# Optimization experiments

Measured on AMD Instinct MI355X. Metric: run time of the kernel, lower is better.

## Reference

```python
import jax, jax.numpy as jnp
import numpy as np

# Module config (matches init_kwargs)
W_BIT = 2
PS_BIT = 8
IC = 256
OC = 256
K = 3
N_XBAR = 576
STRIDE = 1
PAD = 1
NUM_IC = min(IC, N_XBAR // (K * K))   # 64 input channels per crossbar array
GROUPS = IC // NUM_IC                 # 4 arrays (col_slide), ic divides evenly
QP_W = 2 ** W_BIT - 1                 # unsigned levels for nonneg pos/neg weights
QN_PS = -(2 ** (PS_BIT - 1))          # signed psum range
QP_PS = 2 ** (PS_BIT - 1) - 1


def lsq(v, s, qn, qp):
    """LSQ quantize-dequantize with straight-through rounding."""
    vs = jnp.clip(v / s, qn, qp)
    vbar = vs + jax.lax.stop_gradient(jnp.round(vs) - vs)
    return vbar * s


def conv2d(x, w):
    # x: [B, C, H, W], w: [O, C, k, k]
    return jax.lax.conv_general_dilated(
        x, w, window_strides=(STRIDE, STRIDE),
        padding=((PAD, PAD), (PAD, PAD)),
        dimension_numbers=('NCHW', 'OIHW', 'NCHW'))


def setup_inputs() -> dict:
    key = jax.random.key(0)
    k1, k2, k3, k4, k5 = jax.random.split(key, 5)
    x = jax.random.normal(k1, (16, IC, 56, 56), dtype=jnp.float32)
    weight = jax.random.normal(k2, (OC, IC, K, K), dtype=jnp.float32) * 0.05
    # positive LSQ step sizes, roughly 2*E|w|/sqrt(Qp) scale
    w_scale = jax.random.uniform(k3, (GROUPS,), dtype=jnp.float32) * 0.04 + 0.01
    ps_scale_p = jax.random.uniform(k4, (GROUPS,), dtype=jnp.float32) * 0.05 + 0.02
    ps_scale_n = jax.random.uniform(k5, (GROUPS,), dtype=jnp.float32) * 0.05 + 0.02
    return {"x": x, "weight": weight, "w_scale": w_scale,
            "ps_scale_p": ps_scale_p, "ps_scale_n": ps_scale_n}


def reference(x, weight, w_scale, ps_scale_p, ps_scale_n):
    B, _, H, W = x.shape
    # im2col tiling over input channels into GROUPS crossbar arrays
    xg = x.reshape(B, GROUPS, NUM_IC, H, W)                  # [B,G,cg,H,W]
    wg = weight.reshape(OC, GROUPS, NUM_IC, K, K)            # [O,G,cg,k,k]
    # pos / neg weight split, per-array LSQ weight quantization (shared quantizer)
    s_w = w_scale[:, None, None, None, None]                 # [G,1,1,1,1]
    wg_t = jnp.transpose(wg, (1, 0, 2, 3, 4))                # [G,O,cg,k,k]
    wq_p = lsq(jax.nn.relu(wg_t), s_w, 0, QP_W)
    wq_n = lsq(jax.nn.relu(-wg_t), s_w, 0, QP_W)
    xg_t = jnp.transpose(xg, (1, 0, 2, 3, 4))                # [G,B,cg,H,W]
    # per-array partial-sum convs (vmapped over arrays)
    vconv = jax.vmap(conv2d, in_axes=(0, 0))
    psum_p = vconv(xg_t, wq_p)                               # [G,B,O,h,w]
    psum_n = vconv(xg_t, wq_n)
    # per-array psum LSQ quantization ('Array' mode), then accumulate
    s_p = ps_scale_p[:, None, None, None, None]
    s_n = ps_scale_n[:, None, None, None, None]
    out_p = jnp.sum(lsq(psum_p, s_p, QN_PS, QP_PS), axis=0)  # [B,O,h,w]
    out_n = jnp.sum(lsq(psum_n, s_n, QN_PS, QP_PS), axis=0)
    return out_p - out_n
```

## Files before the change

kernel.cpp:

```cpp
#include <hip/hip_runtime.h>
#include <hip/hip_bf16.h>

typedef __attribute__((ext_vector_type(8))) short bf16x8_t;
typedef __attribute__((ext_vector_type(4))) float f32x4_t;
typedef __attribute__((ext_vector_type(4))) unsigned int u32x4_t;

#define XP_BYTES 55115776u
#define WT_BYTES 2359296u

typedef __attribute__((address_space(1))) const unsigned int ga_u32_t;
typedef __attribute__((address_space(3))) unsigned int lds_u32_t;

__device__ __forceinline__ void g2l16(const void* g, void* l) {
  __builtin_amdgcn_global_load_lds((ga_u32_t*)g, (lds_u32_t*)l, 16, 0, 0);
}

__global__ __launch_bounds__(256) void prep_x(const float* __restrict__ x,
                                              __hip_bfloat16* __restrict__ xp) {
  __shared__ float ls[64 * 57];
  int blk = blockIdx.x;
  int g = blk / 896;
  int r = blk - g * 896;
  int b = r / 56;
  int h = r - b * 56;
  int tid = threadIdx.x;
  const float* src = x + (size_t)(b * 256 + g * 64) * 3136 + h * 56;
  for (int i = tid; i < 64 * 56; i += 256) {
    int c = i / 56, w = i - c * 56;
    ls[c * 57 + w] = src[(size_t)c * 3136 + w];
  }
  __syncthreads();
  __hip_bfloat16* gbbase = xp + (size_t)(g * 16 + b) * 58 * 58 * 128;
  __hip_bfloat16* dst = gbbase + ((size_t)(h + 1) * 58 + 1) * 128;
  int wp = tid >> 7;
  int inner = tid & 127;
  int hl = inner >> 6, c = inner & 63;
  for (int w0 = 0; w0 < 56; w0 += 2) {
    int w = w0 + wp;
    float v = ls[c * 57 + w];
    __hip_bfloat16 hi = __float2bfloat16(v);
    __hip_bfloat16 val = hl ? __float2bfloat16(v - __bfloat162float(hi)) : hi;
    dst[(size_t)w * 128 + inner] = val;
  }
  __hip_bfloat16 z = __float2bfloat16(0.0f);
  {
    __hip_bfloat16* rowp = gbbase + (size_t)(h + 1) * 58 * 128;
    if (tid < 128) rowp[inner] = z;
    else           rowp[57 * 128 + inner] = z;
  }
  if (h == 0) {
    for (int i = tid; i < 58 * 128; i += 256) gbbase[i] = z;
  }
  if (h == 55) {
    __hip_bfloat16* r57 = gbbase + (size_t)57 * 58 * 128;
    for (int i = tid; i < 58 * 128; i += 256) r57[i] = z;
  }
}

__global__ __launch_bounds__(256) void prep_w(const float* __restrict__ wgt,
                                              const float* __restrict__ wsc,
                                              unsigned short* __restrict__ wtf) {
  int idx = blockIdx.x * 256 + threadIdx.x;
  if (idx >= 147456) return;
  int l = idx & 63;
  int ni = (idx >> 6) & 3;
  int wq = (idx >> 8) & 3;
  int u = idx >> 10;
  int g = u / 36;
  int r36 = u - g * 36;
  int sgn = (r36 >= 18) ? 1 : 0;
  int r18 = r36 - sgn * 18;
  int tap = r18 >> 1, cc = r18 & 1;
  int oc = wq * 64 + ni * 16 + (l & 15);
  float inv = 1.f / wsc[g];
  unsigned short pk[8];
#pragma unroll
  for (int e = 0; e < 8; ++e) {
    int c = cc * 32 + ((l >> 4) << 3) + e;
    float w = wgt[(size_t)oc * 2304 + (g * 64 + c) * 9 + tap] * inv;
    if (sgn) w = -w;
    float q = rintf(fminf(fmaxf(w, 0.f), 3.f));
    union { __hip_bfloat16 h; unsigned short s; } cv;
    cv.h = __float2bfloat16(q);
    pk[e] = cv.s;
  }
  u32x4_t v;
  v[0] = (unsigned)pk[0] | ((unsigned)pk[1] << 16);
  v[1] = (unsigned)pk[2] | ((unsigned)pk[3] << 16);
  v[2] = (unsigned)pk[4] | ((unsigned)pk[5] << 16);
  v[3] = (unsigned)pk[6] | ((unsigned)pk[7] << 16);
  *(u32x4_t*)(wtf + (size_t)idx * 8) = v;
}

#define MEMPIN asm volatile("" ::: "memory")
#define BAR __builtin_amdgcn_s_barrier()
#define VMCNT0 asm volatile("s_waitcnt vmcnt(0)" ::: "memory")

__global__ __launch_bounds__(256, 2) void conv_mfma(
    const unsigned short* __restrict__ xp, const unsigned short* __restrict__ wtf,
    const float* __restrict__ wsc, const float* __restrict__ psp,
    const float* __restrict__ psn, float* __restrict__ out) {
  __shared__ char Astrip[65536];

  const int bid = blockIdx.x;
  const int wg = (bid & 7) * 98 + (bid >> 3);
  const int b = wg / 49;
  const int t = wg - b * 49;
  const int r0 = (t << 6) / 56;

  const int tid = threadIdx.x;
  const int wv = tid >> 6;
  const int l = tid & 63;

  int pxb[4];
#pragma unroll
  for (int mi = 0; mi < 4; ++mi) {
    int m = (t << 6) + mi * 16 + (l & 15);
    int rv = m / 56, w = m - rv * 56;
    pxb[mi] = ((rv - r0) << 6) + w;
  }

  float w0s = wsc[0], w1s = wsc[1], w2s = wsc[2], w3s = wsc[3];
  float p0 = psp[0], p1 = psp[1], p2 = psp[2], p3 = psp[3];
  float n0 = psn[0], n1 = psn[1], n2 = psn[2], n3 = psn[3];

  f32x4_t acc[4][4], oacc[4][4];
  const f32x4_t fz = {0.f, 0.f, 0.f, 0.f};
#pragma unroll
  for (int i = 0; i < 4; ++i)
#pragma unroll
    for (int j = 0; j < 4; ++j) { acc[i][j] = fz; oacc[i][j] = fz; }

  const char* xg = (const char*)xp;
  const char* wtb = (const char*)wtf + (wv << 12) + (l << 4);
  const unsigned a_gbbase = (unsigned)((b * 3364 + r0 * 58) * 256);

#define STAGE_STRIP(gg)                                                        \
  {                                                                            \
    const char* s_ = xg + (unsigned)(gg)*13778944u + a_gbbase;                 \
    _Pragma("unroll")                                                          \
    for (int k_ = 0; k_ < 16; ++k_) {                                          \
      int idx_ = tid + (k_ << 8);                                              \
      int px_ = idx_ >> 4, sl_ = idx_ & 15;                                    \
      int sr_ = px_ >> 6, xc_ = px_ & 63;                                      \
      g2l16(s_ + (sr_ * 58 + xc_) * 256 +                                      \
                (((sl_ & 8) | ((sl_ & 7) ^ (xc_ & 7))) << 4),                  \
            Astrip + idx_ * 16);                                               \
    }                                                                          \
  }

#define LOADB(d0, d1, d2, d3, uu)                                              \
  {                                                                            \
    const char* p_ = wtb + (unsigned)(uu) * 16384u;                            \
    d0 = *(const bf16x8_t*)(p_);                                               \
    d1 = *(const bf16x8_t*)(p_ + 1024);                                        \
    d2 = *(const bf16x8_t*)(p_ + 2048);                                        \
    d3 = *(const bf16x8_t*)(p_ + 3072);                                        \
  }

#define READA(cc_, tyo_)                                                       \
  {                                                                            \
    const int kj_ = ((cc_) << 2) + (l >> 4);                                   \
    _Pragma("unroll")                                                          \
    for (int mi = 0; mi < 4; ++mi) {                                           \
      int px_ = pxb[mi] + (tyo_);                                              \
      int base_ = (px_ << 8) + ((kj_ ^ (px_ & 7)) << 4);                       \
      ahi[mi] = *(const bf16x8_t*)(Astrip + base_);                            \
      alo[mi] = *(const bf16x8_t*)(Astrip + base_ + 128);                      \
    }                                                                          \
  }

#define MMA32(B0, B1, B2, B3)                                                  \
  __builtin_amdgcn_s_setprio(1);                                               \
  _Pragma("unroll")                                                            \
  for (int mi = 0; mi < 4; ++mi) {                                             \
    acc[mi][0] = __builtin_amdgcn_mfma_f32_16x16x32_bf16(ahi[mi], B0, acc[mi][0], 0, 0, 0); \
    acc[mi][1] = __builtin_amdgcn_mfma_f32_16x16x32_bf16(ahi[mi], B1, acc[mi][1], 0, 0, 0); \
    acc[mi][2] = __builtin_amdgcn_mfma_f32_16x16x32_bf16(ahi[mi], B2, acc[mi][2], 0, 0, 0); \
    acc[mi][3] = __builtin_amdgcn_mfma_f32_16x16x32_bf16(ahi[mi], B3, acc[mi][3], 0, 0, 0); \
  }                                                                            \
  _Pragma("unroll")                                                            \
  for (int mi = 0; mi < 4; ++mi) {                                             \
    acc[mi][0] = __builtin_amdgcn_mfma_f32_16x16x32_bf16(alo[mi], B0, acc[mi][0], 0, 0, 0); \
    acc[mi][1] = __builtin_amdgcn_mfma_f32_16x16x32_bf16(alo[mi], B1, acc[mi][1], 0, 0, 0); \
    acc[mi][2] = __builtin_amdgcn_mfma_f32_16x16x32_bf16(alo[mi], B2, acc[mi][2], 0, 0, 0); \
    acc[mi][3] = __builtin_amdgcn_mfma_f32_16x16x32_bf16(alo[mi], B3, acc[mi][3], 0, 0, 0); \
  }                                                                            \
  __builtin_amdgcn_s_setprio(0);

#define QUANTIZE(gg, ss)                                                       \
  {                                                                            \
    float sw = ((gg) & 2) ? (((gg) & 1) ? w3s : w2s) : (((gg) & 1) ? w1s : w0s); \
    float sp = ((gg) & 2) ? (((gg) & 1) ? p3 : p2) : (((gg) & 1) ? p1 : p0);   \
    float sn = ((gg) & 2) ? (((gg) & 1) ? n3 : n2) : (((gg) & 1) ? n1 : n0);   \
    float sq = (ss) ? sn : sp;                                                 \
    float rs = sw / sq;                                                        \
    float sm = (ss) ? -sq : sq;                                                \
    _Pragma("unroll")                                                          \
    for (int mi = 0; mi < 4; ++mi)                                             \
      _Pragma("unroll")                                                        \
      for (int ni = 0; ni < 4; ++ni)                                           \
        _Pragma("unroll")                                                      \
        for (int j = 0; j < 4; ++j) {                                          \
          float v = acc[mi][ni][j] * rs;                                       \
          v = fminf(fmaxf(v, -128.f), 127.f);                                  \
          oacc[mi][ni][j] += sm * rintf(v);                                    \
          acc[mi][ni][j] = 0.f;                                                \
        }                                                                      \
  }

  bf16x8_t ahi[4], alo[4];
  bf16x8_t bA0, bA1, bA2, bA3, bB0, bB1, bB2, bB3;

  STAGE_STRIP(0);
  MEMPIN;
  LOADB(bA0, bA1, bA2, bA3, 0);
  LOADB(bB0, bB1, bB2, bB3, 1);

  int tap = 0, sgn = 0, g = 0;
  for (int v = 0; v < 72; ++v) {
    const int ty = tap / 3;
    const int tyo = (ty << 6) + (tap - ty * 3);

    if (tap == 0) {
      VMCNT0;
      BAR;
      MEMPIN;
    }

    READA(0, tyo);
    MMA32(bA0, bA1, bA2, bA3);
    if (v < 71) { LOADB(bA0, bA1, bA2, bA3, 2 * v + 2); }

    READA(1, tyo);
    MMA32(bB0, bB1, bB2, bB3);

    if (tap == 8) {
      QUANTIZE(g, sgn);
      if (sgn == 1 && v < 71) {
        BAR;
        MEMPIN;
        STAGE_STRIP(g + 1);
        MEMPIN;
      }
    }
    if (v < 71) { LOADB(bB0, bB1, bB2, bB3, 2 * v + 3); }

    if (++tap == 9) { tap = 0; g += sgn; sgn ^= 1; }
  }

#pragma unroll
  for (int ni = 0; ni < 4; ++ni) {
    int oc = (wv << 6) + ni * 16 + (l & 15);
    float* orow = out + ((size_t)(b * 256 + oc)) * 3136;
#pragma unroll
    for (int mi = 0; mi < 4; ++mi) {
      int m0 = (t << 6) + mi * 16 + ((l >> 4) << 2);
#pragma unroll
      for (int j = 0; j < 4; ++j) {
        orow[m0 + j] = oacc[mi][ni][j];
      }
    }
  }
#undef STAGE_STRIP
#undef LOADB
#undef READA
#undef MMA32
#undef QUANTIZE
}

__global__ __launch_bounds__(256) void naive_conv(
    const float* __restrict__ x, const float* __restrict__ wgt,
    const float* __restrict__ wsc, const float* __restrict__ psp,
    const float* __restrict__ psn, float* __restrict__ out) {
  int idx = blockIdx.x * 256 + threadIdx.x;
  if (idx >= 12845056) return;
  int b = idx / 802816;
  int r = idx - b * 802816;
  int oc = r / 3136;
  int hw = r - oc * 3136;
  int h = hw / 56, w = hw - (hw / 56) * 56;
  float o = 0.f;
  for (int g = 0; g < 4; ++g) {
    float sw = wsc[g];
    float inv = 1.f / sw;
    float pp = 0.f, pn = 0.f;
    for (int tap = 0; tap < 9; ++tap) {
      int y = h + tap / 3 - 1, xx = w + tap % 3 - 1;
      if (y < 0 || y > 55 || xx < 0 || xx > 55) continue;
      const float* xr = x + (size_t)(b * 256 + g * 64) * 3136 + y * 56 + xx;
      const float* wrr = wgt + (size_t)oc * 2304 + (size_t)(g * 64) * 9 + tap;
      for (int c = 0; c < 64; ++c) {
        float xv = xr[(size_t)c * 3136];
        float rv = wrr[c * 9] * inv;
        pp += xv * rintf(fminf(fmaxf(rv, 0.f), 3.f));
        pn += xv * rintf(fminf(fmaxf(-rv, 0.f), 3.f));
      }
    }
    float sp = psp[g], sn = psn[g];
    o += rintf(fminf(fmaxf(pp * (sw / sp), -128.f), 127.f)) * sp;
    o -= rintf(fminf(fmaxf(pn * (sw / sn), -128.f), 127.f)) * sn;
  }
  out[idx] = o;
}

extern "C" void kernel_launch(void* const* d_in, const int* in_sizes, int n_in,
                              void* d_out, int out_size, void* d_ws, size_t ws_size,
                              hipStream_t stream) {
  const float* x = (const float*)d_in[0];
  const float* wgt = (const float*)d_in[1];
  const float* wsc = (const float*)d_in[2];
  const float* psp = (const float*)d_in[3];
  const float* psn = (const float*)d_in[4];
  float* out = (float*)d_out;

  if (ws_size >= (size_t)XP_BYTES + (size_t)WT_BYTES) {
    unsigned short* xpw = (unsigned short*)d_ws;
    unsigned short* wtw = (unsigned short*)((char*)d_ws + XP_BYTES);
    prep_x<<<3584, 256, 0, stream>>>(x, (__hip_bfloat16*)xpw);
    prep_w<<<576, 256, 0, stream>>>(wgt, wsc, wtw);
    conv_mfma<<<784, 256, 0, stream>>>(xpw, wtw, wsc, psp, psn, out);
  } else {
    naive_conv<<<(12845056 + 255) / 256, 256, 0, stream>>>(x, wgt, wsc, psp, psn, out);
  }
}
```

Before: 240.1 us.

## Software-pipeline LDS A-fragment reads behind MFMA sweeps

Splits A-fragment LDS reads into hi and lo halves and interleaves them with 16-MFMA sweeps. Each half is prefetched while the previous half's MFMAs execute, and the next tap's first chunk is loaded ahead of time. Strip staging now waits on lgkm before the barrier and re-reads A after the restage, so the tap-0 barrier no longer sits inside the loop. This aims to hide LDS read latency behind matrix work, at the cost of more live registers and a more fragile ordering between reads and the strip overwrite.

```diff
diff --git a/kernel.cpp b/kernel.cpp
--- a/kernel.cpp
+++ b/kernel.cpp
@@ -95,6 +95,7 @@
 #define MEMPIN asm volatile("" ::: "memory")
 #define BAR __builtin_amdgcn_s_barrier()
 #define VMCNT0 asm volatile("s_waitcnt vmcnt(0)" ::: "memory")
+#define LGKM0 asm volatile("s_waitcnt lgkmcnt(0)" ::: "memory")
 
 __global__ __launch_bounds__(256, 2) void conv_mfma(
     const unsigned short* __restrict__ xp, const unsigned short* __restrict__ wtf,
@@ -158,33 +159,36 @@
     d3 = *(const bf16x8_t*)(p_ + 3072);                                        \
   }
 
-#define READA(cc_, tyo_)                                                       \
+#define READA_HI(cc_, tyo_)                                                    \
   {                                                                            \
     const int kj_ = ((cc_) << 2) + (l >> 4);                                   \
     _Pragma("unroll")                                                          \
     for (int mi = 0; mi < 4; ++mi) {                                           \
       int px_ = pxb[mi] + (tyo_);                                              \
-      int base_ = (px_ << 8) + ((kj_ ^ (px_ & 7)) << 4);                       \
-      ahi[mi] = *(const bf16x8_t*)(Astrip + base_);                            \
-      alo[mi] = *(const bf16x8_t*)(Astrip + base_ + 128);                      \
+      ahi[mi] = *(const bf16x8_t*)(Astrip + (px_ << 8) +                       \
+                                   ((kj_ ^ (px_ & 7)) << 4));                  \
     }                                                                          \
   }
 
-#define MMA32(B0, B1, B2, B3)                                                  \
+#define READA_LO(cc_, tyo_)                                                    \
+  {                                                                            \
+    const int kj_ = ((cc_) << 2) + (l >> 4);                                   \
+    _Pragma("unroll")                                                          \
+    for (int mi = 0; mi < 4; ++mi) {                                           \
+      int px_ = pxb[mi] + (tyo_);                                              \
+      alo[mi] = *(const bf16x8_t*)(Astrip + (px_ << 8) +                       \
+                                   ((kj_ ^ (px_ & 7)) << 4) + 128);            \
+    }                                                                          \
+  }
+
+#define SWEEP16(AF, B0, B1, B2, B3)                                            \
   __builtin_amdgcn_s_setprio(1);                                               \
   _Pragma("unroll")                                                            \
   for (int mi = 0; mi < 4; ++mi) {                                             \
-    acc[mi][0] = __builtin_amdgcn_mfma_f32_16x16x32_bf16(ahi[mi], B0, acc[mi][0], 0, 0, 0); \
-    acc[mi][1] = __builtin_amdgcn_mfma_f32_16x16x32_bf16(ahi[mi], B1, acc[mi][1], 0, 0, 0); \
-    acc[mi][2] = __builtin_amdgcn_mfma_f32_16x16x32_bf16(ahi[mi], B2, acc[mi][2], 0, 0, 0); \
-    acc[mi][3] = __builtin_amdgcn_mfma_f32_16x16x32_bf16(ahi[mi], B3, acc[mi][3], 0, 0, 0); \
-  }                                                                            \
-  _Pragma("unroll")                                                            \
-  for (int mi = 0; mi < 4; ++mi) {                                             \
-    acc[mi][0] = __builtin_amdgcn_mfma_f32_16x16x32_bf16(alo[mi], B0, acc[mi][0], 0, 0, 0); \
-    acc[mi][1] = __builtin_amdgcn_mfma_f32_16x16x32_bf16(alo[mi], B1, acc[mi][1], 0, 0, 0); \
-    acc[mi][2] = __builtin_amdgcn_mfma_f32_16x16x32_bf16(alo[mi], B2, acc[mi][2], 0, 0, 0); \
-    acc[mi][3] = __builtin_amdgcn_mfma_f32_16x16x32_bf16(alo[mi], B3, acc[mi][3], 0, 0, 0); \
+    acc[mi][0] = __builtin_amdgcn_mfma_f32_16x16x32_bf16(AF[mi], B0, acc[mi][0], 0, 0, 0); \
+    acc[mi][1] = __builtin_amdgcn_mfma_f32_16x16x32_bf16(AF[mi], B1, acc[mi][1], 0, 0, 0); \
+    acc[mi][2] = __builtin_amdgcn_mfma_f32_16x16x32_bf16(AF[mi], B2, acc[mi][2], 0, 0, 0); \
+    acc[mi][3] = __builtin_amdgcn_mfma_f32_16x16x32_bf16(AF[mi], B3, acc[mi][3], 0, 0, 0); \
   }                                                                            \
   __builtin_amdgcn_s_setprio(0);
 
@@ -216,32 +220,48 @@
   MEMPIN;
   LOADB(bA0, bA1, bA2, bA3, 0);
   LOADB(bB0, bB1, bB2, bB3, 1);
+  VMCNT0;
+  BAR;
+  MEMPIN;
+  READA_HI(0, 0);
+  READA_LO(0, 0);
 
   int tap = 0, sgn = 0, g = 0;
   for (int v = 0; v < 72; ++v) {
     const int ty = tap / 3;
     const int tyo = (ty << 6) + (tap - ty * 3);
-
-    if (tap == 0) {
-      VMCNT0;
-      BAR;
-      MEMPIN;
-    }
-
-    READA(0, tyo);
-    MMA32(bA0, bA1, bA2, bA3);
+    const int tapN = (tap < 8) ? (tap + 1) : 0;
+    const int tyN = tapN / 3;
+    const int tyoN = (tyN << 6) + (tapN - tyN * 3);
+
+    SWEEP16(ahi, bA0, bA1, bA2, bA3);
+    READA_HI(1, tyo);
+    SWEEP16(alo, bA0, bA1, bA2, bA3);
+    READA_LO(1, tyo);
     if (v < 71) { LOADB(bA0, bA1, bA2, bA3, 2 * v + 2); }
 
-    READA(1, tyo);
-    MMA32(bB0, bB1, bB2, bB3);
+    SWEEP16(ahi, bB0, bB1, bB2, bB3);
+    if (tap < 8) { READA_HI(0, tyoN); }
+    SWEEP16(alo, bB0, bB1, bB2, bB3);
+    if (tap < 8) { READA_LO(0, tyoN); }
 
     if (tap == 8) {
       QUANTIZE(g, sgn);
-      if (sgn == 1 && v < 71) {
-        BAR;
-        MEMPIN;
-        STAGE_STRIP(g + 1);
-        MEMPIN;
+      if (v < 71) {
+        if (sgn == 0) {
+          READA_HI(0, 0);
+          READA_LO(0, 0);
+        } else {
+          LGKM0;
+          BAR;
+          MEMPIN;
+          STAGE_STRIP(g + 1);
+          VMCNT0;
+          BAR;
+          MEMPIN;
+          READA_HI(0, 0);
+          READA_LO(0, 0);
+        }
       }
     }
     if (v < 71) { LOADB(bB0, bB1, bB2, bB3, 2 * v + 3); }
@@ -264,8 +284,9 @@
   }
 #undef STAGE_STRIP
 #undef LOADB
-#undef READA
-#undef MMA32
+#undef READA_HI
+#undef READA_LO
+#undef SWEEP16
 #undef QUANTIZE
 }
 
```

Result: slower. 272.2 us (+13.4%).
